# Kernel tuning notes

Hardware: AMD Instinct MI355X
Metric: run time of the kernel (lower is better)

## Reference

```python
import jax, jax.numpy as jnp
import numpy as np

BETA = 5.0
B, D, K, E2 = 64, 3072, 512, 64


def setup_inputs() -> dict:
    key = jax.random.key(0)
    k1, k2, k3, k4 = jax.random.split(key, 4)
    images = jax.random.normal(k1, (B, D), dtype=jnp.float32)
    w_proj = jax.random.normal(k2, (K, D), dtype=jnp.float32) * 0.02   # project.weight
    w_img2 = jax.random.normal(k3, (K, D * E2), dtype=jnp.float32) * 0.02  # img2.weight
    w_rec = jax.random.normal(k4, (E2, K), dtype=jnp.float32) * 0.02   # rec.weight
    return {"images": images, "w_proj": w_proj, "w_img2": w_img2, "w_rec": w_rec}


def reference(images, w_proj, w_img2, w_rec):
    beta = BETA
    wimg = w_proj.T            # (D, K)
    wrec = w_rec.T             # (K, E2)
    # img2.weight (K, D*E2) -> codebook tensor (K, D, E2), std-normalized over D (ddof=1 to match torch)
    wimg2 = w_img2.reshape(K, D, E2)
    wimg2 = wimg2 / (0.01 + jnp.std(wimg2, axis=1, keepdims=True, ddof=1))

    # ---- encode ----
    xd = images[:, :, None] - wimg[None]          # (B, D, K)
    xh = -jnp.mean(xd * xd, axis=1) * beta        # (B, K)
    xp = jax.nn.softmax(xh, axis=-1)              # (B, K)
    lat1 = xp @ wrec                              # (B, E2)
    xe = jnp.einsum('bdk,kde->bke', xd, wimg2)    # (B, K, E2)
    lat2 = jnp.einsum('bke,bk->be', xe, xp)       # (B, E2)

    # ---- decode ----
    diff = lat1[:, :, None] - wrec.T[None]        # (B, E2, K); wrec.T is (E2, K)
    xh2 = -jnp.mean(diff * diff, axis=1) * beta   # (B, K)
    xp2 = jax.nn.softmax(xh2, axis=-1)            # (B, K)
    xx = xp2[:, :, None] * lat2[:, None, :]       # (B, K, E2)
    xd2 = jnp.einsum('bke,kde->bd', xx, wimg2)    # (B, D)
    images_recon = xp2 @ wimg.T + xd2             # (B, D)

    loss = jnp.mean((images_recon - images) ** 2, axis=-1)  # (B,)
    return loss
```

## Files before the change

kernel.cpp:

```cpp
#include <hip/hip_runtime.h>
#include <math.h>

#define Bn 64
#define Dn 3072
#define Kn 512
#define En 64

static constexpr float BETA = 5.0f;

static constexpr size_t XE_OFF    = 0;
static constexpr size_t S_OFF     = 2097152;
static constexpr size_t DOT_OFF   = 2129920;
static constexpr size_t NPROJ_OFF = 2162688;
static constexpr size_t XP_OFF    = 2163200;
static constexpr size_t LAT1_OFF  = 2195968;
static constexpr size_t LAT2_OFF  = 2200064;
static constexpr size_t XP2_OFF   = 2204160;
static constexpr size_t WRECT_OFF = 2236928;
static constexpr size_t FRAG_OFF  = 2269696;
static constexpr size_t PART_OFF  = 2269696;

typedef float  f4  __attribute__((ext_vector_type(4)));
typedef __bf16 bf8 __attribute__((ext_vector_type(8)));
typedef int    i4  __attribute__((ext_vector_type(4)));

union AB { i4 i; bf8 b; };

__device__ __forceinline__ unsigned short bf16b(float x) {
  __bf16 h = (__bf16)x;
  union Cv { __bf16 h; unsigned short u; } c;
  c.h = h;
  return c.u;
}

__device__ __forceinline__ float waveAllMax(float v) {
#pragma unroll
  for (int o = 32; o; o >>= 1) v = fmaxf(v, __shfl_xor(v, o));
  return v;
}
__device__ __forceinline__ float waveAllSum(float v) {
#pragma unroll
  for (int o = 32; o; o >>= 1) v += __shfl_xor(v, o);
  return v;
}

__global__ __launch_bounds__(256) void kPrep(const float* __restrict__ img,
                                             float* __restrict__ ws) {
  const int t = threadIdx.x, ds = blockIdx.x;
  const int T = t >> 6, l = t & 63;
  const int b = 16 * T + (l & 15);
  const int d0 = 32 * ds + 8 * (l >> 4);
  const float* p = img + (size_t)b * Dn + d0;
  unsigned short u[8];
#pragma unroll
  for (int j = 0; j < 8; ++j) u[j] = bf16b(p[j]);
  i4 v;
  v.x = (int)u[0] | ((int)u[1] << 16);
  v.y = (int)u[2] | ((int)u[3] << 16);
  v.z = (int)u[4] | ((int)u[5] << 16);
  v.w = (int)u[6] | ((int)u[7] << 16);
  ((i4*)(ws + FRAG_OFF))[(ds * 4 + T) * 64 + l] = v;
}

__global__ __launch_bounds__(256) void kTr(const float* __restrict__ wrec, float* __restrict__ ws) {
  int g = blockIdx.x * 256 + threadIdx.x;
  int k = g >> 6, e = g & 63;
  ws[WRECT_OFF + g] = wrec[(size_t)e * Kn + k];
}

__global__ __launch_bounds__(256) void kDot(const float* __restrict__ wproj,
                                            float* __restrict__ ws) {
  const int t = threadIdx.x, w = t >> 6, l = t & 63, elane = l & 15, dgrp = l >> 4;
  const int kk = blockIdx.x * 16 + elane;
  const i4* afr = (const i4*)(ws + FRAG_OFF);
  const float* wrow = wproj + (size_t)kk * Dn;
  f4 acc = {0.f, 0.f, 0.f, 0.f};
  float np = 0.f;
  float bwA[8], bwB[8];
  i4 avA, avB;
  avA = afr[(0 * 4 + w) * 64 + l];
#pragma unroll
  for (int j = 0; j < 8; ++j) bwA[j] = wrow[8 * dgrp + j];

#define KD_ITER(BWC, BWN, AVC, AVN, N) {                                         \
    const int np1 = (N) + 1;                                                     \
    if (np1 < 96) {                                                              \
      AVN = afr[(np1 * 4 + w) * 64 + l];                                         \
      _Pragma("unroll")                                                          \
      for (int j = 0; j < 8; ++j) BWN[j] = wrow[(size_t)np1 * 32 + 8 * dgrp + j];\
    }                                                                            \
    bf8 bfr;                                                                     \
    _Pragma("unroll")                                                            \
    for (int j = 0; j < 8; ++j) { float v = BWC[j]; np = fmaf(v, v, np); bfr[j] = (__bf16)v; } \
    AB a; a.i = AVC;                                                             \
    acc = __builtin_amdgcn_mfma_f32_16x16x32_bf16(a.b, bfr, acc, 0, 0, 0);       \
  }

  for (int n = 0; n < 96; n += 2) {
    KD_ITER(bwA, bwB, avA, avB, n)
    KD_ITER(bwB, bwA, avB, avA, n + 1)
  }
#undef KD_ITER
#pragma unroll
  for (int r = 0; r < 4; ++r) {
    int b = 16 * w + 4 * dgrp + r;
    ws[DOT_OFF + (size_t)b * Kn + kk] = acc[r];
  }
  np += __shfl_xor(np, 16);
  np += __shfl_xor(np, 32);
  if (w == 0 && dgrp == 0) ws[NPROJ_OFF + kk] = np;
}

__global__ __launch_bounds__(256) void kA(const float* __restrict__ wproj,
                                          const float* __restrict__ w2,
                                          float* __restrict__ ws) {
  const int k = blockIdx.x, t = threadIdx.x;
  const int w = t >> 6, l = t & 63, elane = l & 15, dgrp = l >> 4;
  const int ecol = 16 * w + elane;
  __shared__ float wp[Dn];
  const float* wpk = wproj + (size_t)k * Dn;
#pragma unroll
  for (int i = 0; i < 3; ++i) ((f4*)wp)[t + 256 * i] = ((const f4*)wpk)[t + 256 * i];
  __syncthreads();

  const i4* afr = (const i4*)(ws + FRAG_OFF);
  const float* w2k = w2 + (size_t)k * (Dn * En);
  f4 acc0 = {0.f,0.f,0.f,0.f}, acc1 = {0.f,0.f,0.f,0.f};
  f4 acc2 = {0.f,0.f,0.f,0.f}, acc3 = {0.f,0.f,0.f,0.f};
  float ssum = 0.f, ssq = 0.f, pacc = 0.f;
  float bwA[8], bwB[8];
  i4 avA[4], avB[4];
#pragma unroll
  for (int j = 0; j < 8; ++j) bwA[j] = w2k[(size_t)(8 * dgrp + j) * 64 + ecol];
#pragma unroll
  for (int T = 0; T < 4; ++T) avA[T] = afr[T * 64 + l];

#define KA_ITER(BWC, BWN, AVC, AVN, N) {                                         \
    const int np1 = (N) + 1;                                                     \
    if (np1 < 96) {                                                              \
      _Pragma("unroll")                                                          \
      for (int j = 0; j < 8; ++j)                                                \
        BWN[j] = w2k[(size_t)(np1 * 32 + 8 * dgrp + j) * 64 + ecol];             \
      _Pragma("unroll")                                                          \
      for (int T = 0; T < 4; ++T) AVN[T] = afr[(np1 * 4 + T) * 64 + l];          \
    }                                                                            \
    bf8 bfr;                                                                     \
    _Pragma("unroll")                                                            \
    for (int j = 0; j < 8; ++j) {                                                \
      float v = BWC[j];                                                          \
      ssum += v; ssq = fmaf(v, v, ssq);                                          \
      pacc = fmaf(wp[(N) * 32 + 8 * dgrp + j], v, pacc);                         \
      bfr[j] = (__bf16)v;                                                        \
    }                                                                            \
    AB a0, a1, a2, a3;                                                           \
    a0.i = AVC[0]; a1.i = AVC[1]; a2.i = AVC[2]; a3.i = AVC[3];                  \
    acc0 = __builtin_amdgcn_mfma_f32_16x16x32_bf16(a0.b, bfr, acc0, 0, 0, 0);    \
    acc1 = __builtin_amdgcn_mfma_f32_16x16x32_bf16(a1.b, bfr, acc1, 0, 0, 0);    \
    acc2 = __builtin_amdgcn_mfma_f32_16x16x32_bf16(a2.b, bfr, acc2, 0, 0, 0);    \
    acc3 = __builtin_amdgcn_mfma_f32_16x16x32_bf16(a3.b, bfr, acc3, 0, 0, 0);    \
  }

  for (int n = 0; n < 96; n += 2) {
    KA_ITER(bwA, bwB, avA, avB, n)
    KA_ITER(bwB, bwA, avB, avA, n + 1)
  }
#undef KA_ITER

  ssum += __shfl_xor(ssum, 16); ssum += __shfl_xor(ssum, 32);
  ssq  += __shfl_xor(ssq, 16);  ssq  += __shfl_xor(ssq, 32);
  pacc += __shfl_xor(pacc, 16); pacc += __shfl_xor(pacc, 32);
  float var = (ssq - ssum * ssum * (1.0f / Dn)) * (1.0f / (Dn - 1));
  float sv = 1.0f / (0.01f + sqrtf(fmaxf(var, 0.f)));
  if (dgrp == 0) ws[S_OFF + (size_t)k * En + ecol] = sv;
#pragma unroll
  for (int T = 0; T < 4; ++T) {
    f4 a = (T == 0) ? acc0 : (T == 1) ? acc1 : (T == 2) ? acc2 : acc3;
#pragma unroll
    for (int r = 0; r < 4; ++r) {
      int b = 16 * T + 4 * dgrp + r;
      ws[XE_OFF + ((size_t)b * Kn + k) * En + ecol] = sv * (a[r] - pacc);
    }
  }
}

__global__ __launch_bounds__(256) void kMid1(const float* __restrict__ img,
                                             float* __restrict__ ws) {
  const int b = blockIdx.x;
  const int t = threadIdx.x;
  const int wid = t >> 6, lane = t & 63;
  __shared__ float xp_sh[512];
  __shared__ float red[16];
  __shared__ float scratch[256];

  float acc = 0.f;
  const f4* irow = (const f4*)(img + (size_t)b * Dn);
#pragma unroll
  for (int i = 0; i < 3; ++i) {
    f4 v = irow[t + 256 * i];
    acc = fmaf(v.x, v.x, acc); acc = fmaf(v.y, v.y, acc);
    acc = fmaf(v.z, v.z, acc); acc = fmaf(v.w, v.w, acc);
  }
  acc = waveAllSum(acc);
  if (lane == 0) red[wid] = acc;
  __syncthreads();
  const float nimg = red[0] + red[1] + red[2] + red[3];

  const float c = -(BETA / Dn);
  float d1 = ws[DOT_OFF + (size_t)b * Kn + t];
  float d2 = ws[DOT_OFF + (size_t)b * Kn + t + 256];
  float np1 = ws[NPROJ_OFF + t];
  float np2 = ws[NPROJ_OFF + t + 256];
  float x1 = c * (nimg - 2.f * d1 + np1);
  float x2 = c * (nimg - 2.f * d2 + np2);

  float m = waveAllMax(fmaxf(x1, x2));
  if (lane == 0) red[4 + wid] = m;
  __syncthreads();
  m = fmaxf(fmaxf(red[4], red[5]), fmaxf(red[6], red[7]));
  float e1 = expf(x1 - m), e2 = expf(x2 - m);
  float sv = waveAllSum(e1 + e2);
  if (lane == 0) red[8 + wid] = sv;
  __syncthreads();
  float inv = 1.f / (red[8] + red[9] + red[10] + red[11]);
  float p1 = e1 * inv, p2 = e2 * inv;
  xp_sh[t] = p1; xp_sh[t + 256] = p2;
  ws[XP_OFF + (size_t)b * Kn + t] = p1;
  ws[XP_OFF + (size_t)b * Kn + t + 256] = p2;
  __syncthreads();

  const int e = t & 63, q = t >> 6;
  float lacc = 0.f;
  for (int kk = q * 128; kk < q * 128 + 128; ++kk)
    lacc = fmaf(xp_sh[kk], ws[WRECT_OFF + (size_t)kk * En + e], lacc);
  scratch[q * 64 + e] = lacc;
  __syncthreads();
  if (t < 64)
    ws[LAT1_OFF + (size_t)b * En + t] =
        scratch[t] + scratch[64 + t] + scratch[128 + t] + scratch[192 + t];
}

__global__ __launch_bounds__(256) void kMid2(float* __restrict__ ws) {
  const int b = blockIdx.x;
  const int t = threadIdx.x;
  const int wid = t >> 6, lane = t & 63;
  __shared__ float xp_sh[512];
  __shared__ __align__(16) float l1_sh[64];
  __shared__ float scratch[256];
  __shared__ float red[16];

  xp_sh[t] = ws[XP_OFF + (size_t)b * Kn + t];
  xp_sh[t + 256] = ws[XP_OFF + (size_t)b * Kn + t + 256];
  if (t < 64) l1_sh[t] = ws[LAT1_OFF + (size_t)b * En + t];
  __syncthreads();

  const int e = t & 63, q = t >> 6;
  const float* xeb = ws + XE_OFF + (size_t)b * Kn * En;
  float lacc = 0.f;
  for (int kk = q * 128; kk < q * 128 + 128; ++kk)
    lacc = fmaf(xp_sh[kk], xeb[(size_t)kk * En + e], lacc);
  scratch[q * 64 + e] = lacc;
  __syncthreads();
  if (t < 64)
    ws[LAT2_OFF + (size_t)b * En + t] =
        scratch[t] + scratch[64 + t] + scratch[128 + t] + scratch[192 + t];

  float h1 = 0.f, h2 = 0.f;
#pragma unroll
  for (int i = 0; i < 16; ++i) {
    f4 lv = *(const f4*)&l1_sh[i * 4];
    f4 w1 = *(const f4*)&ws[WRECT_OFF + (size_t)t * En + i * 4];
    f4 w2v = *(const f4*)&ws[WRECT_OFF + ((size_t)t + 256) * En + i * 4];
    float a0 = lv.x - w1.x, a1 = lv.y - w1.y, a2 = lv.z - w1.z, a3 = lv.w - w1.w;
    h1 = fmaf(a0, a0, h1); h1 = fmaf(a1, a1, h1);
    h1 = fmaf(a2, a2, h1); h1 = fmaf(a3, a3, h1);
    float b0 = lv.x - w2v.x, b1 = lv.y - w2v.y, b2 = lv.z - w2v.z, b3 = lv.w - w2v.w;
    h2 = fmaf(b0, b0, h2); h2 = fmaf(b1, b1, h2);
    h2 = fmaf(b2, b2, h2); h2 = fmaf(b3, b3, h2);
  }
  const float c2 = -(BETA / En);
  float x1 = c2 * h1, x2 = c2 * h2;

  float m = waveAllMax(fmaxf(x1, x2));
  if (lane == 0) red[4 + wid] = m;
  __syncthreads();
  m = fmaxf(fmaxf(red[4], red[5]), fmaxf(red[6], red[7]));
  float e1 = expf(x1 - m), e2 = expf(x2 - m);
  float sv = waveAllSum(e1 + e2);
  if (lane == 0) red[8 + wid] = sv;
  __syncthreads();
  float inv = 1.f / (red[8] + red[9] + red[10] + red[11]);
  float p1 = e1 * inv, p2 = e2 * inv;
  ws[XP2_OFF + (size_t)b * Kn + t] = p1;
  ws[XP2_OFF + (size_t)b * Kn + t + 256] = p2;
  unsigned short* xpb = (unsigned short*)(ws + DOT_OFF);
  xpb[(size_t)b * Kn + t] = bf16b(p1);
  xpb[(size_t)b * Kn + t + 256] = bf16b(p2);
}

__global__ __launch_bounds__(256) void kZ(float* __restrict__ ws) {
  const int g = blockIdx.x * 256 + threadIdx.x;
  const int S = g >> 8;
  const int T = (g >> 6) & 3;
  const int l = g & 63;
  const int dgrp = l >> 4;
  const int b = 16 * T + (l & 15);
  const int kd0 = S * 32 + 8 * dgrp;
  const int k = kd0 >> 6;
  const int e0 = kd0 & 63;
  const float xp2v = ws[XP2_OFF + (size_t)b * Kn + k];
  unsigned short u[8];
#pragma unroll
  for (int j = 0; j < 8; ++j) {
    float v = xp2v * ws[LAT2_OFF + (size_t)b * En + e0 + j] * ws[S_OFF + (size_t)k * En + e0 + j];
    u[j] = bf16b(v);
  }
  i4 v;
  v.x = (int)u[0] | ((int)u[1] << 16);
  v.y = (int)u[2] | ((int)u[3] << 16);
  v.z = (int)u[4] | ((int)u[5] << 16);
  v.w = (int)u[6] | ((int)u[7] << 16);
  ((i4*)(ws + XE_OFF))[g] = v;
}

__global__ __launch_bounds__(256) void kB(const float* __restrict__ wproj,
                                          const float* __restrict__ w2,
                                          float* __restrict__ ws) {
  const int dtile = blockIdx.x, ks = blockIdx.y, t = threadIdx.x;
  const int w = t >> 6, l = t & 63, elane = l & 15, dgrp = l >> 4;
  const int d = dtile * 64 + 16 * w + elane;
  const i4* zfr = (const i4*)(ws + XE_OFF);
  f4 acc0 = {0.f,0.f,0.f,0.f}, acc1 = {0.f,0.f,0.f,0.f};
  f4 acc2 = {0.f,0.f,0.f,0.f}, acc3 = {0.f,0.f,0.f,0.f};
  f4 bwA[2], bwB[2];
  i4 avA[4], avB[4];
  {
    const f4* p = (const f4*)(w2 + ((size_t)(ks * 32) * Dn + d) * En + 8 * dgrp);
    bwA[0] = p[0]; bwA[1] = p[1];
#pragma unroll
    for (int T = 0; T < 4; ++T) avA[T] = zfr[((ks * 64) * 4 + T) * 64 + l];
  }

#define KB_ITER(BWC, BWN, AVC, AVN, N) {                                         \
    const int np1 = (N) + 1;                                                     \
    if (np1 < 64) {                                                              \
      const int kk = ks * 32 + (np1 >> 1);                                       \
      const int e0 = (np1 & 1) * 32;                                             \
      const f4* p = (const f4*)(w2 + ((size_t)kk * Dn + d) * En + e0 + 8 * dgrp);\
      BWN[0] = p[0]; BWN[1] = p[1];                                              \
      _Pragma("unroll")                                                          \
      for (int T = 0; T < 4; ++T) AVN[T] = zfr[((ks * 64 + np1) * 4 + T) * 64 + l]; \
    }                                                                            \
    bf8 bfr;                                                                     \
    _Pragma("unroll")                                                            \
    for (int j = 0; j < 4; ++j) {                                                \
      bfr[j] = (__bf16)BWC[0][j];                                                \
      bfr[4 + j] = (__bf16)BWC[1][j];                                            \
    }                                                                            \
    AB a0, a1, a2, a3;                                                           \
    a0.i = AVC[0]; a1.i = AVC[1]; a2.i = AVC[2]; a3.i = AVC[3];                  \
    acc0 = __builtin_amdgcn_mfma_f32_16x16x32_bf16(a0.b, bfr, acc0, 0, 0, 0);    \
    acc1 = __builtin_amdgcn_mfma_f32_16x16x32_bf16(a1.b, bfr, acc1, 0, 0, 0);    \
    acc2 = __builtin_amdgcn_mfma_f32_16x16x32_bf16(a2.b, bfr, acc2, 0, 0, 0);    \
    acc3 = __builtin_amdgcn_mfma_f32_16x16x32_bf16(a3.b, bfr, acc3, 0, 0, 0);    \
  }

  for (int n = 0; n < 64; n += 2) {
    KB_ITER(bwA, bwB, avA, avB, n)
    KB_ITER(bwB, bwA, avB, avA, n + 1)
  }
#undef KB_ITER

  {
    const int kk0 = ks * 32;
    bf8 bw;
#pragma unroll
    for (int j = 0; j < 8; ++j)
      bw[j] = (__bf16)wproj[(size_t)(kk0 + 8 * dgrp + j) * Dn + d];
    const unsigned short* xpb = (const unsigned short*)(ws + DOT_OFF);
    AB a0, a1, a2, a3;
    a0.i = *(const i4*)&xpb[(size_t)(0 * 16 + elane) * Kn + kk0 + 8 * dgrp];
    a1.i = *(const i4*)&xpb[(size_t)(1 * 16 + elane) * Kn + kk0 + 8 * dgrp];
    a2.i = *(const i4*)&xpb[(size_t)(2 * 16 + elane) * Kn + kk0 + 8 * dgrp];
    a3.i = *(const i4*)&xpb[(size_t)(3 * 16 + elane) * Kn + kk0 + 8 * dgrp];
    acc0 = __builtin_amdgcn_mfma_f32_16x16x32_bf16(a0.b, bw, acc0, 0, 0, 0);
    acc1 = __builtin_amdgcn_mfma_f32_16x16x32_bf16(a1.b, bw, acc1, 0, 0, 0);
    acc2 = __builtin_amdgcn_mfma_f32_16x16x32_bf16(a2.b, bw, acc2, 0, 0, 0);
    acc3 = __builtin_amdgcn_mfma_f32_16x16x32_bf16(a3.b, bw, acc3, 0, 0, 0);
  }

#pragma unroll
  for (int T = 0; T < 4; ++T) {
    f4 a = (T == 0) ? acc0 : (T == 1) ? acc1 : (T == 2) ? acc2 : acc3;
#pragma unroll
    for (int r = 0; r < 4; ++r) {
      int b = 16 * T + 4 * dgrp + r;
      ws[PART_OFF + ((size_t)ks * Bn + b) * Dn + d] = a[r];
    }
  }
}

__global__ __launch_bounds__(256) void kLoss(const float* __restrict__ img,
                                             const float* __restrict__ ws,
                                             float* __restrict__ out) {
  const int b = blockIdx.x, t = threadIdx.x;
  __shared__ float red[4];
  float acc = 0.f;
  const f4* p4 = (const f4*)(ws + PART_OFF);
  const f4* i4p = (const f4*)(img + (size_t)b * Dn);
  const int rowq = Dn / 4;
#pragma unroll
  for (int i = 0; i < 3; ++i) {
    int idx = t + 256 * i;
    f4 r = {0.f, 0.f, 0.f, 0.f};
#pragma unroll
    for (int s = 0; s < 16; ++s)
      r += p4[((size_t)s * Bn + b) * rowq + idx];
    f4 v = i4p[idx];
    float dx = r.x - v.x, dy = r.y - v.y, dz = r.z - v.z, dw = r.w - v.w;
    acc = fmaf(dx, dx, acc); acc = fmaf(dy, dy, acc);
    acc = fmaf(dz, dz, acc); acc = fmaf(dw, dw, acc);
  }
  acc = waveAllSum(acc);
  if ((t & 63) == 0) red[t >> 6] = acc;
  __syncthreads();
  if (t == 0) out[b] = (red[0] + red[1] + red[2] + red[3]) * (1.0f / Dn);
}

extern "C" void kernel_launch(void* const* d_in, const int* in_sizes, int n_in,
                              void* d_out, int out_size, void* d_ws, size_t ws_size,
                              hipStream_t stream) {
  const float* img   = (const float*)d_in[0];
  const float* wproj = (const float*)d_in[1];
  const float* w2    = (const float*)d_in[2];
  const float* wrec  = (const float*)d_in[3];
  float* ws  = (float*)d_ws;
  float* out = (float*)d_out;

  hipLaunchKernelGGL(kPrep,  dim3(96),  dim3(256), 0, stream, img, ws);
  hipLaunchKernelGGL(kTr,    dim3(128), dim3(256), 0, stream, wrec, ws);
  hipLaunchKernelGGL(kDot,   dim3(32),  dim3(256), 0, stream, wproj, ws);
  hipLaunchKernelGGL(kA,     dim3(512), dim3(256), 0, stream, wproj, w2, ws);
  hipLaunchKernelGGL(kMid1,  dim3(64),  dim3(256), 0, stream, img, ws);
  hipLaunchKernelGGL(kMid2,  dim3(64),  dim3(256), 0, stream, ws);
  hipLaunchKernelGGL(kZ,     dim3(1024),dim3(256), 0, stream, ws);
  hipLaunchKernelGGL(kB,     dim3(48, 16), dim3(256), 0, stream, wproj, w2, ws);
  hipLaunchKernelGGL(kLoss,  dim3(64),  dim3(256), 0, stream, img, ws, out);
}
```

Measured before the change: 262.2 us.

## Split D reduction in kA and kDot across blocks, merge prep and mid kernels

The dot-product kernel now splits the D reduction into 8 chunks and kA into 2 halves, writing partial accumulators and partial statistics to workspace. A new kStat kernel combines the std statistics, and kMid (merging kMid1 and kMid2) sums the partials while computing lat2. kPrep and kTr are fused into one launch. kA stops double-buffering its A fragments to save registers, and occupancy hints are added. The aim is more blocks in flight for the small dot kernel and the big kA pass, plus fewer launches. In exchange it adds extra partial-sum traffic through workspace and an extra small kernel.

Measured after the change: 254.6 us. 2.9% less time.

```diff
diff --git a/kernel.cpp b/kernel.cpp
--- a/kernel.cpp
+++ b/kernel.cpp
@@ -8,17 +8,19 @@
 
 static constexpr float BETA = 5.0f;
 
-static constexpr size_t XE_OFF    = 0;
-static constexpr size_t S_OFF     = 2097152;
-static constexpr size_t DOT_OFF   = 2129920;
-static constexpr size_t NPROJ_OFF = 2162688;
-static constexpr size_t XP_OFF    = 2163200;
-static constexpr size_t LAT1_OFF  = 2195968;
-static constexpr size_t LAT2_OFF  = 2200064;
-static constexpr size_t XP2_OFF   = 2204160;
-static constexpr size_t WRECT_OFF = 2236928;
-static constexpr size_t FRAG_OFF  = 2269696;
-static constexpr size_t PART_OFF  = 2269696;
+static constexpr size_t ZF_OFF    = 0;
+static constexpr size_t ACCP_OFF  = 1048576;
+static constexpr size_t PART_OFF  = 1048576;
+static constexpr size_t STATP_OFF = 5242880;
+static constexpr size_t S_OFF     = 5439488;
+static constexpr size_t PACC_OFF  = 5472256;
+static constexpr size_t DOTP_OFF  = 5505024;
+static constexpr size_t NPP_OFF   = 5767168;
+static constexpr size_t XP2_OFF   = 5771264;
+static constexpr size_t XP2B_OFF  = 5804032;
+static constexpr size_t LAT2_OFF  = 5820416;
+static constexpr size_t WRECT_OFF = 5824512;
+static constexpr size_t FRAG_OFF  = 5857280;
 
 typedef float  f4  __attribute__((ext_vector_type(4)));
 typedef __bf16 bf8 __attribute__((ext_vector_type(8)));
@@ -44,50 +46,55 @@
   return v;
 }
 
-__global__ __launch_bounds__(256) void kPrep(const float* __restrict__ img,
+__global__ __launch_bounds__(256) void kPT(const float* __restrict__ img,
+                                           const float* __restrict__ wrec,
+                                           float* __restrict__ ws) {
+  const int t = threadIdx.x;
+  if (blockIdx.x < 96) {
+    const int ds = blockIdx.x;
+    const int T = t >> 6, l = t & 63;
+    const int b = 16 * T + (l & 15);
+    const int d0 = 32 * ds + 8 * (l >> 4);
+    const float* p = img + (size_t)b * Dn + d0;
+    unsigned short u[8];
+#pragma unroll
+    for (int j = 0; j < 8; ++j) u[j] = bf16b(p[j]);
+    i4 v;
+    v.x = (int)u[0] | ((int)u[1] << 16);
+    v.y = (int)u[2] | ((int)u[3] << 16);
+    v.z = (int)u[4] | ((int)u[5] << 16);
+    v.w = (int)u[6] | ((int)u[7] << 16);
+    ((i4*)(ws + FRAG_OFF))[(ds * 4 + T) * 64 + l] = v;
+  } else {
+    int g = (blockIdx.x - 96) * 256 + t;
+    int k = g >> 6, e = g & 63;
+    ws[WRECT_OFF + g] = wrec[(size_t)e * Kn + k];
+  }
+}
+
+__global__ __launch_bounds__(256) void kDotP(const float* __restrict__ wproj,
                                              float* __restrict__ ws) {
-  const int t = threadIdx.x, ds = blockIdx.x;
-  const int T = t >> 6, l = t & 63;
-  const int b = 16 * T + (l & 15);
-  const int d0 = 32 * ds + 8 * (l >> 4);
-  const float* p = img + (size_t)b * Dn + d0;
-  unsigned short u[8];
-#pragma unroll
-  for (int j = 0; j < 8; ++j) u[j] = bf16b(p[j]);
-  i4 v;
-  v.x = (int)u[0] | ((int)u[1] << 16);
-  v.y = (int)u[2] | ((int)u[3] << 16);
-  v.z = (int)u[4] | ((int)u[5] << 16);
-  v.w = (int)u[6] | ((int)u[7] << 16);
-  ((i4*)(ws + FRAG_OFF))[(ds * 4 + T) * 64 + l] = v;
-}
-
-__global__ __launch_bounds__(256) void kTr(const float* __restrict__ wrec, float* __restrict__ ws) {
-  int g = blockIdx.x * 256 + threadIdx.x;
-  int k = g >> 6, e = g & 63;
-  ws[WRECT_OFF + g] = wrec[(size_t)e * Kn + k];
-}
-
-__global__ __launch_bounds__(256) void kDot(const float* __restrict__ wproj,
-                                            float* __restrict__ ws) {
   const int t = threadIdx.x, w = t >> 6, l = t & 63, elane = l & 15, dgrp = l >> 4;
   const int kk = blockIdx.x * 16 + elane;
+  const int dc = blockIdx.y;
+  const int n0 = dc * 12;
   const i4* afr = (const i4*)(ws + FRAG_OFF);
   const float* wrow = wproj + (size_t)kk * Dn;
   f4 acc = {0.f, 0.f, 0.f, 0.f};
   float np = 0.f;
   float bwA[8], bwB[8];
   i4 avA, avB;
-  avA = afr[(0 * 4 + w) * 64 + l];
-#pragma unroll
-  for (int j = 0; j < 8; ++j) bwA[j] = wrow[8 * dgrp + j];
-
-#define KD_ITER(BWC, BWN, AVC, AVN, N) {                                         \
-    const int np1 = (N) + 1;                                                     \
-    if (np1 < 96) {                                                              \
-      AVN = afr[(np1 * 4 + w) * 64 + l];                                         \
+  avA = afr[((size_t)n0 * 4 + w) * 64 + l];
+#pragma unroll
+  for (int j = 0; j < 8; ++j) bwA[j] = wrow[(size_t)n0 * 32 + 8 * dgrp + j];
+
+#define KD_ITER(BWC, BWN, AVC, AVN, NL) {                                        \
+    const int nl1 = (NL) + 1;                                                    \
+    if (nl1 < 12) {                                                              \
+      AVN = afr[((size_t)(n0 + nl1) * 4 + w) * 64 + l];                          \
       _Pragma("unroll")                                                          \
-      for (int j = 0; j < 8; ++j) BWN[j] = wrow[(size_t)np1 * 32 + 8 * dgrp + j];\
+      for (int j = 0; j < 8; ++j)                                                \
+        BWN[j] = wrow[(size_t)(n0 + nl1) * 32 + 8 * dgrp + j];                   \
     }                                                                            \
     bf8 bfr;                                                                     \
     _Pragma("unroll")                                                            \
@@ -96,31 +103,36 @@
     acc = __builtin_amdgcn_mfma_f32_16x16x32_bf16(a.b, bfr, acc, 0, 0, 0);       \
   }
 
-  for (int n = 0; n < 96; n += 2) {
-    KD_ITER(bwA, bwB, avA, avB, n)
-    KD_ITER(bwB, bwA, avB, avA, n + 1)
+  for (int nl = 0; nl < 12; nl += 2) {
+    KD_ITER(bwA, bwB, avA, avB, nl)
+    KD_ITER(bwB, bwA, avB, avA, nl + 1)
   }
 #undef KD_ITER
 #pragma unroll
   for (int r = 0; r < 4; ++r) {
     int b = 16 * w + 4 * dgrp + r;
-    ws[DOT_OFF + (size_t)b * Kn + kk] = acc[r];
+    ws[DOTP_OFF + (size_t)dc * (Bn * Kn) + (size_t)b * Kn + kk] = acc[r];
   }
   np += __shfl_xor(np, 16);
   np += __shfl_xor(np, 32);
-  if (w == 0 && dgrp == 0) ws[NPROJ_OFF + kk] = np;
-}
-
-__global__ __launch_bounds__(256) void kA(const float* __restrict__ wproj,
-                                          const float* __restrict__ w2,
-                                          float* __restrict__ ws) {
-  const int k = blockIdx.x, t = threadIdx.x;
+  if (w == 0 && dgrp == 0) ws[NPP_OFF + (size_t)dc * Kn + kk] = np;
+}
+
+__global__ __launch_bounds__(256, 4) void kA(const float* __restrict__ wproj,
+                                             const float* __restrict__ w2,
+                                             float* __restrict__ ws) {
+  const int k = blockIdx.x, h = blockIdx.y, t = threadIdx.x;
   const int w = t >> 6, l = t & 63, elane = l & 15, dgrp = l >> 4;
   const int ecol = 16 * w + elane;
-  __shared__ float wp[Dn];
-  const float* wpk = wproj + (size_t)k * Dn;
-#pragma unroll
-  for (int i = 0; i < 3; ++i) ((f4*)wp)[t + 256 * i] = ((const f4*)wpk)[t + 256 * i];
+  const int n0 = h * 48;
+  __shared__ float wp[Dn / 2];
+  const float* wpk = wproj + (size_t)k * Dn + (size_t)h * (Dn / 2);
+  {
+    f4* dst = (f4*)wp;
+    const f4* src = (const f4*)wpk;
+    dst[t] = src[t];
+    if (t < 128) dst[t + 256] = src[t + 256];
+  }
   __syncthreads();
 
   const i4* afr = (const i4*)(ws + FRAG_OFF);
@@ -129,68 +141,85 @@
   f4 acc2 = {0.f,0.f,0.f,0.f}, acc3 = {0.f,0.f,0.f,0.f};
   float ssum = 0.f, ssq = 0.f, pacc = 0.f;
   float bwA[8], bwB[8];
-  i4 avA[4], avB[4];
-#pragma unroll
-  for (int j = 0; j < 8; ++j) bwA[j] = w2k[(size_t)(8 * dgrp + j) * 64 + ecol];
-#pragma unroll
-  for (int T = 0; T < 4; ++T) avA[T] = afr[T * 64 + l];
-
-#define KA_ITER(BWC, BWN, AVC, AVN, N) {                                         \
-    const int np1 = (N) + 1;                                                     \
-    if (np1 < 96) {                                                              \
+#pragma unroll
+  for (int j = 0; j < 8; ++j)
+    bwA[j] = w2k[(size_t)(n0 * 32 + 8 * dgrp + j) * 64 + ecol];
+
+#define KA_ITER(BWC, BWN, NL) {                                                  \
+    const int nl1 = (NL) + 1;                                                    \
+    if (nl1 < 48) {                                                              \
       _Pragma("unroll")                                                          \
       for (int j = 0; j < 8; ++j)                                                \
-        BWN[j] = w2k[(size_t)(np1 * 32 + 8 * dgrp + j) * 64 + ecol];             \
-      _Pragma("unroll")                                                          \
-      for (int T = 0; T < 4; ++T) AVN[T] = afr[(np1 * 4 + T) * 64 + l];          \
+        BWN[j] = w2k[(size_t)((n0 + nl1) * 32 + 8 * dgrp + j) * 64 + ecol];      \
     }                                                                            \
+    i4 av0 = afr[((size_t)(n0 + (NL)) * 4 + 0) * 64 + l];                        \
+    i4 av1 = afr[((size_t)(n0 + (NL)) * 4 + 1) * 64 + l];                        \
+    i4 av2 = afr[((size_t)(n0 + (NL)) * 4 + 2) * 64 + l];                        \
+    i4 av3 = afr[((size_t)(n0 + (NL)) * 4 + 3) * 64 + l];                        \
     bf8 bfr;                                                                     \
     _Pragma("unroll")                                                            \
     for (int j = 0; j < 8; ++j) {                                                \
       float v = BWC[j];                                                          \
       ssum += v; ssq = fmaf(v, v, ssq);                                          \
-      pacc = fmaf(wp[(N) * 32 + 8 * dgrp + j], v, pacc);                         \
+      pacc = fmaf(wp[(NL) * 32 + 8 * dgrp + j], v, pacc);                        \
       bfr[j] = (__bf16)v;                                                        \
     }                                                                            \
     AB a0, a1, a2, a3;                                                           \
-    a0.i = AVC[0]; a1.i = AVC[1]; a2.i = AVC[2]; a3.i = AVC[3];                  \
+    a0.i = av0; a1.i = av1; a2.i = av2; a3.i = av3;                              \
     acc0 = __builtin_amdgcn_mfma_f32_16x16x32_bf16(a0.b, bfr, acc0, 0, 0, 0);    \
     acc1 = __builtin_amdgcn_mfma_f32_16x16x32_bf16(a1.b, bfr, acc1, 0, 0, 0);    \
     acc2 = __builtin_amdgcn_mfma_f32_16x16x32_bf16(a2.b, bfr, acc2, 0, 0, 0);    \
     acc3 = __builtin_amdgcn_mfma_f32_16x16x32_bf16(a3.b, bfr, acc3, 0, 0, 0);    \
   }
 
-  for (int n = 0; n < 96; n += 2) {
-    KA_ITER(bwA, bwB, avA, avB, n)
-    KA_ITER(bwB, bwA, avB, avA, n + 1)
+  for (int nl = 0; nl < 48; nl += 2) {
+    KA_ITER(bwA, bwB, nl)
+    KA_ITER(bwB, bwA, nl + 1)
   }
 #undef KA_ITER
 
   ssum += __shfl_xor(ssum, 16); ssum += __shfl_xor(ssum, 32);
   ssq  += __shfl_xor(ssq, 16);  ssq  += __shfl_xor(ssq, 32);
   pacc += __shfl_xor(pacc, 16); pacc += __shfl_xor(pacc, 32);
+  const size_t kh = (size_t)(k * 2 + h);
+  if (dgrp == 0) {
+    ws[STATP_OFF + kh * 192 + 0 * 64 + ecol] = ssum;
+    ws[STATP_OFF + kh * 192 + 1 * 64 + ecol] = ssq;
+    ws[STATP_OFF + kh * 192 + 2 * 64 + ecol] = pacc;
+  }
+#pragma unroll
+  for (int T = 0; T < 4; ++T) {
+    f4 a = (T == 0) ? acc0 : (T == 1) ? acc1 : (T == 2) ? acc2 : acc3;
+#pragma unroll
+    for (int r = 0; r < 4; ++r) {
+      int b = 16 * T + 4 * dgrp + r;
+      ws[ACCP_OFF + kh * 4096 + (size_t)b * 64 + ecol] = a[r];
+    }
+  }
+}
+
+__global__ __launch_bounds__(64) void kStat(float* __restrict__ ws) {
+  const int k = blockIdx.x, e = threadIdx.x;
+  const size_t o0 = STATP_OFF + (size_t)(2 * k) * 192;
+  const size_t o1 = STATP_OFF + (size_t)(2 * k + 1) * 192;
+  float ssum = ws[o0 + e] + ws[o1 + e];
+  float ssq  = ws[o0 + 64 + e] + ws[o1 + 64 + e];
+  float pacc = ws[o0 + 128 + e] + ws[o1 + 128 + e];
   float var = (ssq - ssum * ssum * (1.0f / Dn)) * (1.0f / (Dn - 1));
   float sv = 1.0f / (0.01f + sqrtf(fmaxf(var, 0.f)));
-  if (dgrp == 0) ws[S_OFF + (size_t)k * En + ecol] = sv;
-#pragma unroll
-  for (int T = 0; T < 4; ++T) {
-    f4 a = (T == 0) ? acc0 : (T == 1) ? acc1 : (T == 2) ? acc2 : acc3;
-#pragma unroll
-    for (int r = 0; r < 4; ++r) {
-      int b = 16 * T + 4 * dgrp + r;
-      ws[XE_OFF + ((size_t)b * Kn + k) * En + ecol] = sv * (a[r] - pacc);
-    }
-  }
-}
-
-__global__ __launch_bounds__(256) void kMid1(const float* __restrict__ img,
-                                             float* __restrict__ ws) {
+  ws[S_OFF + (size_t)k * 64 + e] = sv;
+  ws[PACC_OFF + (size_t)k * 64 + e] = pacc;
+}
+
+__global__ __launch_bounds__(256) void kMid(const float* __restrict__ img,
+                                            float* __restrict__ ws) {
   const int b = blockIdx.x;
   const int t = threadIdx.x;
   const int wid = t >> 6, lane = t & 63;
   __shared__ float xp_sh[512];
   __shared__ float red[16];
   __shared__ float scratch[256];
+  __shared__ __align__(16) float l1_sh[64];
 
   float acc = 0.f;
   const f4* irow = (const f4*)(img + (size_t)b * Dn);
@@ -205,13 +234,17 @@
   __syncthreads();
   const float nimg = red[0] + red[1] + red[2] + red[3];
 
+  float d1 = 0.f, d2 = 0.f, npa = 0.f, npb = 0.f;
+#pragma unroll
+  for (int dc = 0; dc < 8; ++dc) {
+    d1  += ws[DOTP_OFF + (size_t)dc * (Bn * Kn) + (size_t)b * Kn + t];
+    d2  += ws[DOTP_OFF + (size_t)dc * (Bn * Kn) + (size_t)b * Kn + t + 256];
+    npa += ws[NPP_OFF + (size_t)dc * Kn + t];
+    npb += ws[NPP_OFF + (size_t)dc * Kn + t + 256];
+  }
   const float c = -(BETA / Dn);
-  float d1 = ws[DOT_OFF + (size_t)b * Kn + t];
-  float d2 = ws[DOT_OFF + (size_t)b * Kn + t + 256];
-  float np1 = ws[NPROJ_OFF + t];
-  float np2 = ws[NPROJ_OFF + t + 256];
-  float x1 = c * (nimg - 2.f * d1 + np1);
-  float x2 = c * (nimg - 2.f * d2 + np2);
+  float x1 = c * (nimg - 2.f * d1 + npa);
+  float x2 = c * (nimg - 2.f * d2 + npb);
 
   float m = waveAllMax(fmaxf(x1, x2));
   if (lane == 0) red[4 + wid] = m;
@@ -222,10 +255,8 @@
   if (lane == 0) red[8 + wid] = sv;
   __syncthreads();
   float inv = 1.f / (red[8] + red[9] + red[10] + red[11]);
-  float p1 = e1 * inv, p2 = e2 * inv;
-  xp_sh[t] = p1; xp_sh[t + 256] = p2;
-  ws[XP_OFF + (size_t)b * Kn + t] = p1;
-  ws[XP_OFF + (size_t)b * Kn + t + 256] = p2;
+  xp_sh[t] = e1 * inv;
+  xp_sh[t + 256] = e2 * inv;
   __syncthreads();
 
   const int e = t & 63, q = t >> 6;
@@ -235,30 +266,18 @@
   scratch[q * 64 + e] = lacc;
   __syncthreads();
   if (t < 64)
-    ws[LAT1_OFF + (size_t)b * En + t] =
-        scratch[t] + scratch[64 + t] + scratch[128 + t] + scratch[192 + t];
-}
-
-__global__ __launch_bounds__(256) void kMid2(float* __restrict__ ws) {
-  const int b = blockIdx.x;
-  const int t = threadIdx.x;
-  const int wid = t >> 6, lane = t & 63;
-  __shared__ float xp_sh[512];
-  __shared__ __align__(16) float l1_sh[64];
-  __shared__ float scratch[256];
-  __shared__ float red[16];
-
-  xp_sh[t] = ws[XP_OFF + (size_t)b * Kn + t];
-  xp_sh[t + 256] = ws[XP_OFF + (size_t)b * Kn + t + 256];
-  if (t < 64) l1_sh[t] = ws[LAT1_OFF + (size_t)b * En + t];
-  __syncthreads();
-
-  const int e = t & 63, q = t >> 6;
-  const float* xeb = ws + XE_OFF + (size_t)b * Kn * En;
-  float lacc = 0.f;
-  for (int kk = q * 128; kk < q * 128 + 128; ++kk)
-    lacc = fmaf(xp_sh[kk], xeb[(size_t)kk * En + e], lacc);
-  scratch[q * 64 + e] = lacc;
+    l1_sh[t] = scratch[t] + scratch[64 + t] + scratch[128 + t] + scratch[192 + t];
+  __syncthreads();
+
+  float l2acc = 0.f;
+  for (int kk = q * 128; kk < q * 128 + 128; ++kk) {
+    float a = ws[ACCP_OFF + (size_t)(2 * kk) * 4096 + (size_t)b * 64 + e]
+            + ws[ACCP_OFF + (size_t)(2 * kk + 1) * 4096 + (size_t)b * 64 + e];
+    l2acc = fmaf(xp_sh[kk] * ws[S_OFF + (size_t)kk * 64 + e],
+                 a - ws[PACC_OFF + (size_t)kk * 64 + e], l2acc);
+  }
+  __syncthreads();
+  scratch[q * 64 + e] = l2acc;
   __syncthreads();
   if (t < 64)
     ws[LAT2_OFF + (size_t)b * En + t] =
@@ -278,21 +297,21 @@
     h2 = fmaf(b2, b2, h2); h2 = fmaf(b3, b3, h2);
   }
   const float c2 = -(BETA / En);
-  float x1 = c2 * h1, x2 = c2 * h2;
-
-  float m = waveAllMax(fmaxf(x1, x2));
+  x1 = c2 * h1; x2 = c2 * h2;
+
+  m = waveAllMax(fmaxf(x1, x2));
   if (lane == 0) red[4 + wid] = m;
   __syncthreads();
   m = fmaxf(fmaxf(red[4], red[5]), fmaxf(red[6], red[7]));
-  float e1 = expf(x1 - m), e2 = expf(x2 - m);
-  float sv = waveAllSum(e1 + e2);
+  e1 = expf(x1 - m); e2 = expf(x2 - m);
+  sv = waveAllSum(e1 + e2);
   if (lane == 0) red[8 + wid] = sv;
   __syncthreads();
-  float inv = 1.f / (red[8] + red[9] + red[10] + red[11]);
+  inv = 1.f / (red[8] + red[9] + red[10] + red[11]);
   float p1 = e1 * inv, p2 = e2 * inv;
   ws[XP2_OFF + (size_t)b * Kn + t] = p1;
   ws[XP2_OFF + (size_t)b * Kn + t + 256] = p2;
-  unsigned short* xpb = (unsigned short*)(ws + DOT_OFF);
+  unsigned short* xpb = (unsigned short*)(ws + XP2B_OFF);
   xpb[(size_t)b * Kn + t] = bf16b(p1);
   xpb[(size_t)b * Kn + t + 256] = bf16b(p2);
 }
@@ -319,16 +338,16 @@
   v.y = (int)u[2] | ((int)u[3] << 16);
   v.z = (int)u[4] | ((int)u[5] << 16);
   v.w = (int)u[6] | ((int)u[7] << 16);
-  ((i4*)(ws + XE_OFF))[g] = v;
-}
-
-__global__ __launch_bounds__(256) void kB(const float* __restrict__ wproj,
-                                          const float* __restrict__ w2,
-                                          float* __restrict__ ws) {
+  ((i4*)(ws + ZF_OFF))[g] = v;
+}
+
+__global__ __launch_bounds__(256, 3) void kB(const float* __restrict__ wproj,
+                                             const float* __restrict__ w2,
+                                             float* __restrict__ ws) {
   const int dtile = blockIdx.x, ks = blockIdx.y, t = threadIdx.x;
   const int w = t >> 6, l = t & 63, elane = l & 15, dgrp = l >> 4;
   const int d = dtile * 64 + 16 * w + elane;
-  const i4* zfr = (const i4*)(ws + XE_OFF);
+  const i4* zfr = (const i4*)(ws + ZF_OFF);
   f4 acc0 = {0.f,0.f,0.f,0.f}, acc1 = {0.f,0.f,0.f,0.f};
   f4 acc2 = {0.f,0.f,0.f,0.f}, acc3 = {0.f,0.f,0.f,0.f};
   f4 bwA[2], bwB[2];
@@ -337,7 +356,7 @@
     const f4* p = (const f4*)(w2 + ((size_t)(ks * 32) * Dn + d) * En + 8 * dgrp);
     bwA[0] = p[0]; bwA[1] = p[1];
 #pragma unroll
-    for (int T = 0; T < 4; ++T) avA[T] = zfr[((ks * 64) * 4 + T) * 64 + l];
+    for (int T = 0; T < 4; ++T) avA[T] = zfr[((size_t)(ks * 64) * 4 + T) * 64 + l];
   }
 
 #define KB_ITER(BWC, BWN, AVC, AVN, N) {                                         \
@@ -348,7 +367,8 @@
       const f4* p = (const f4*)(w2 + ((size_t)kk * Dn + d) * En + e0 + 8 * dgrp);\
       BWN[0] = p[0]; BWN[1] = p[1];                                              \
       _Pragma("unroll")                                                          \
-      for (int T = 0; T < 4; ++T) AVN[T] = zfr[((ks * 64 + np1) * 4 + T) * 64 + l]; \
+      for (int T = 0; T < 4; ++T)                                                \
+        AVN[T] = zfr[((size_t)(ks * 64 + np1) * 4 + T) * 64 + l];                \
     }                                                                            \
     bf8 bfr;                                                                     \
     _Pragma("unroll")                                                            \
@@ -376,7 +396,7 @@
 #pragma unroll
     for (int j = 0; j < 8; ++j)
       bw[j] = (__bf16)wproj[(size_t)(kk0 + 8 * dgrp + j) * Dn + d];
-    const unsigned short* xpb = (const unsigned short*)(ws + DOT_OFF);
+    const unsigned short* xpb = (const unsigned short*)(ws + XP2B_OFF);
     AB a0, a1, a2, a3;
     a0.i = *(const i4*)&xpb[(size_t)(0 * 16 + elane) * Kn + kk0 + 8 * dgrp];
     a1.i = *(const i4*)&xpb[(size_t)(1 * 16 + elane) * Kn + kk0 + 8 * dgrp];
@@ -436,13 +456,12 @@
   float* ws  = (float*)d_ws;
   float* out = (float*)d_out;
 
-  hipLaunchKernelGGL(kPrep,  dim3(96),  dim3(256), 0, stream, img, ws);
-  hipLaunchKernelGGL(kTr,    dim3(128), dim3(256), 0, stream, wrec, ws);
-  hipLaunchKernelGGL(kDot,   dim3(32),  dim3(256), 0, stream, wproj, ws);
-  hipLaunchKernelGGL(kA,     dim3(512), dim3(256), 0, stream, wproj, w2, ws);
-  hipLaunchKernelGGL(kMid1,  dim3(64),  dim3(256), 0, stream, img, ws);
-  hipLaunchKernelGGL(kMid2,  dim3(64),  dim3(256), 0, stream, ws);
-  hipLaunchKernelGGL(kZ,     dim3(1024),dim3(256), 0, stream, ws);
-  hipLaunchKernelGGL(kB,     dim3(48, 16), dim3(256), 0, stream, wproj, w2, ws);
-  hipLaunchKernelGGL(kLoss,  dim3(64),  dim3(256), 0, stream, img, ws, out);
-}
+  hipLaunchKernelGGL(kPT,   dim3(224), dim3(256), 0, stream, img, wrec, ws);
+  hipLaunchKernelGGL(kDotP, dim3(32, 8), dim3(256), 0, stream, wproj, ws);
+  hipLaunchKernelGGL(kA,    dim3(512, 2), dim3(256), 0, stream, wproj, w2, ws);
+  hipLaunchKernelGGL(kStat, dim3(512), dim3(64), 0, stream, ws);
+  hipLaunchKernelGGL(kMid,  dim3(64),  dim3(256), 0, stream, img, ws);
+  hipLaunchKernelGGL(kZ,    dim3(1024), dim3(256), 0, stream, ws);
+  hipLaunchKernelGGL(kB,    dim3(48, 16), dim3(256), 0, stream, wproj, w2, ws);
+  hipLaunchKernelGGL(kLoss, dim3(64),  dim3(256), 0, stream, img, ws, out);
+}
```
